# Performance work log

Hardware: AMD Instinct MI355X
Metric: run time of the kernel (lower is better)

## Reference

```python
import jax, jax.numpy as jnp
import numpy as np

N = 10000        # nodes
E = 160000       # edges (avg degree 16)
IN = 8 * 144     # 1152
OUT = 2 * 144    # 288 per ChebConv
KS = [4, 5, 6, 7]


def setup_inputs() -> dict:
    key = jax.random.key(0)
    ks = jax.random.split(key, 10)
    x = jax.random.normal(ks[0], (N, IN), dtype=jnp.float32)
    edge_index = jax.random.randint(ks[1], (2, E), 0, N, dtype=jnp.int32)
    d = {"x": x, "edge_index": edge_index}
    for i, (name, K) in enumerate(zip(["3", "5", "7", "9"], KS)):
        d["W" + name] = jax.random.normal(ks[2 + i], (K, IN, OUT), dtype=jnp.float32) * 0.02
        d["b" + name] = jnp.zeros((OUT,), dtype=jnp.float32)
    return d


def _cheb_basis(x, edge_index, K):
    """Chebyshev basis T_0..T_{K-1} of L_hat = -D^{-1/2} A D^{-1/2} (lambda_max=2,
    as in PyG ChebConv default; self-loop term 2/lambda_max - 1 = 0)."""
    row, col = edge_index[0], edge_index[1]  # source, target
    n = x.shape[0]
    w = jnp.ones(row.shape, x.dtype)
    deg = jax.ops.segment_sum(w, row, num_segments=n)
    dinv = jnp.where(deg > 0, jax.lax.rsqrt(jnp.maximum(deg, 1e-12)), 0.0)
    norm = -(dinv[row] * dinv[col])  # [E]

    def prop(h):  # out[i] = sum_{j->i} norm_e * h[j]
        return jax.ops.segment_sum(h[row] * norm[:, None], col, num_segments=n)

    Tx = [x, prop(x)]
    for _ in range(K - 2):
        Tx.append(2.0 * prop(Tx[-1]) - Tx[-2])
    return jnp.stack(Tx[:K], axis=0)  # [K, N, F]


def reference(x, edge_index, W3, b3, W5, b5, W7, b7, W9, b9):
    T = _cheb_basis(x, edge_index, max(KS))  # shared basis; identical math per conv
    outs = []
    for W, b in ((W3, b3), (W5, b5), (W7, b7), (W9, b9)):
        K = W.shape[0]
        outs.append(jnp.einsum('knf,kfo->no', T[:K], W) + b)
    return jnp.concatenate(outs, axis=1)  # [N, 4*OUT]
```

## Files before the change

### kernel.cpp

```cpp
#include <hip/hip_runtime.h>

#define NN 10000
#define NE 160000
#define FIN 1152
#define FOUT 288
#define FOUT_TOTAL 1152
#define NF (NN * FOUT)
#define WSL (FIN * FOUT)
#define NSLICE 22

typedef __attribute__((ext_vector_type(8))) short short8;
typedef __attribute__((ext_vector_type(8))) unsigned short ushort8v;
typedef __attribute__((ext_vector_type(4))) float floatx4;

__device__ __forceinline__ unsigned short f2bf(float f) {
  unsigned int u = __float_as_uint(f);
  u += 0x7FFF + ((u >> 16) & 1);
  return (unsigned short)(u >> 16);
}
__device__ __forceinline__ float bf2f(unsigned short u) {
  return __uint_as_float(((unsigned int)u) << 16);
}

__device__ __forceinline__ void async_copy16(void* lds, const void* gmem) {
  __builtin_amdgcn_global_load_lds(
      (const __attribute__((address_space(1))) unsigned int*)gmem,
      (__attribute__((address_space(3))) unsigned int*)lds, 16, 0, 0);
}


__global__ void deg_kernel(const int* __restrict__ ei, int* __restrict__ deg,
                           int* __restrict__ indeg) {
  int e = blockIdx.x * 256 + threadIdx.x;
  if (e < NE) {
    atomicAdd(&deg[ei[e]], 1);
    atomicAdd(&indeg[ei[NE + e]], 1);
  }
}

__global__ void dinv_kernel(const int* __restrict__ deg, float* __restrict__ dinv) {
  int i = blockIdx.x * 256 + threadIdx.x;
  if (i < NN) {
    int d = deg[i];
    dinv[i] = d > 0 ? rsqrtf((float)d) : 0.0f;
  }
}

__global__ void scan_kernel(const int* __restrict__ indeg, int* __restrict__ rowptr,
                            int* __restrict__ cursor) {
  __shared__ int s[256];
  __shared__ int carry_s;
  if (threadIdx.x == 0) carry_s = 0;
  __syncthreads();
  for (int base = 0; base < NN; base += 256) {
    int i = base + threadIdx.x;
    int v = (i < NN) ? indeg[i] : 0;
    s[threadIdx.x] = v;
    __syncthreads();
    for (int off = 1; off < 256; off <<= 1) {
      int t = (threadIdx.x >= off) ? s[threadIdx.x - off] : 0;
      __syncthreads();
      s[threadIdx.x] += t;
      __syncthreads();
    }
    int excl = s[threadIdx.x] - v + carry_s;
    if (i < NN) { rowptr[i] = excl; cursor[i] = excl; }
    __syncthreads();
    if (threadIdx.x == 0) carry_s += s[255];
    __syncthreads();
  }
  if (threadIdx.x == 0) rowptr[NN] = carry_s;
}

__global__ void scatter_kernel(const int* __restrict__ ei, const float* __restrict__ dinv,
                               int* __restrict__ cursor, int* __restrict__ srcarr,
                               float* __restrict__ wn) {
  int e = blockIdx.x * 256 + threadIdx.x;
  if (e < NE) {
    int r = ei[e], c = ei[NE + e];
    int pos = atomicAdd(&cursor[c], 1);
    srcarr[pos] = r;
    wn[pos] = -(dinv[r] * dinv[c]);
  }
}

__global__ void wtrans_kernel(const float* __restrict__ W0, const float* __restrict__ W1,
                              const float* __restrict__ W2, const float* __restrict__ W3,
                              unsigned short* __restrict__ Wt) {
  int i = blockIdx.x * 256 + threadIdx.x;
  if (i >= NSLICE * WSL) return;
  int s = i / WSL;
  int rem = i - s * WSL;
  int o = rem / FIN;
  int f = rem - o * FIN;
  int c, k;
  if (s < 4)       { c = 0; k = s; }
  else if (s < 9)  { c = 1; k = s - 4; }
  else if (s < 15) { c = 2; k = s - 9; }
  else             { c = 3; k = s - 15; }
  const float* W = (c == 0) ? W0 : (c == 1) ? W1 : (c == 2) ? W2 : W3;
  Wt[i] = f2bf(W[(size_t)k * WSL + (size_t)f * FOUT + o]);
}

__global__ void xcast_kernel(const float* __restrict__ x, unsigned short* __restrict__ xb) {
  int i = blockIdx.x * 256 + threadIdx.x;
  if (i < NN * FIN / 4) {
    float4 v = *(const float4*)(x + (size_t)i * 4);
    ushort4 r;
    r.x = f2bf(v.x); r.y = f2bf(v.y); r.z = f2bf(v.z); r.w = f2bf(v.w);
    *(ushort4*)(xb + (size_t)i * 4) = r;
  }
}

__global__ __launch_bounds__(256) void gemm_mfma_kernel(
    const unsigned short* __restrict__ Xb, const unsigned short* __restrict__ Wt,
    unsigned short* __restrict__ Yall) {
  const int bx = blockIdx.x;
  const int slice = bx / 3;
  const int n0 = (bx - slice * 3) * 96;
  const int m0 = blockIdx.y * 128;

  __shared__ unsigned short As[128][64];
  __shared__ unsigned short Bs[96][64];

  const int tid = threadIdx.x;
  const int lane = tid & 63;
  const int wave = tid >> 6;
  const int wx = wave & 1;
  const int wy = wave >> 1;
  const int lm = lane & 15;
  const int lkb = (lane >> 4) * 8;

  floatx4 acc[4][3];
#pragma unroll
  for (int i = 0; i < 4; i++)
#pragma unroll
    for (int j = 0; j < 3; j++) acc[i][j] = (floatx4){0.f, 0.f, 0.f, 0.f};

  const unsigned short* Wbase = Wt + (size_t)slice * WSL;

  for (int f0 = 0; f0 < FIN; f0 += 64) {
    __syncthreads();
#pragma unroll
    for (int i = 0; i < 4; i++) {
      int idx = i * 256 + tid;
      int row = idx >> 3;
      int cb = (idx & 7) * 16;
      int gr = m0 + row;
      gr = gr < NN ? gr : NN - 1;
      async_copy16((char*)&As[0][0] + idx * 16,
                   (const char*)Xb + ((size_t)gr * FIN + f0) * 2 + cb);
    }
#pragma unroll
    for (int i = 0; i < 3; i++) {
      int idx = i * 256 + tid;
      int row = idx >> 3;
      int cb = (idx & 7) * 16;
      async_copy16((char*)&Bs[0][0] + idx * 16,
                   (const char*)Wbase + ((size_t)(n0 + row) * FIN + f0) * 2 + cb);
    }
    __syncthreads();
#pragma unroll
    for (int s = 0; s < 2; s++) {
      short8 a[4], b[3];
#pragma unroll
      for (int i = 0; i < 4; i++)
        a[i] = *(const short8*)&As[wy * 64 + i * 16 + lm][s * 32 + lkb];
#pragma unroll
      for (int j = 0; j < 3; j++)
        b[j] = *(const short8*)&Bs[wx * 48 + j * 16 + lm][s * 32 + lkb];
#pragma unroll
      for (int i = 0; i < 4; i++)
#pragma unroll
        for (int j = 0; j < 3; j++)
          acc[i][j] = __builtin_amdgcn_mfma_f32_16x16x32_bf16(a[i], b[j], acc[i][j], 0, 0, 0);
    }
  }
  unsigned short* Yb = Yall + (size_t)slice * NF;
  const int cbase = n0 + wx * 48 + lm;
  const int rbase = (lane >> 4) * 4;
#pragma unroll
  for (int i = 0; i < 4; i++) {
#pragma unroll
    for (int r = 0; r < 4; r++) {
      int grow = m0 + wy * 64 + i * 16 + rbase + r;
      if (grow < NN) {
        unsigned short* op = Yb + (size_t)grow * FOUT + cbase;
#pragma unroll
        for (int j = 0; j < 3; j++) op[j * 16] = f2bf(acc[i][j][r]);
      }
    }
  }
}


struct StepArgs {
  const unsigned short* H[4];
  const unsigned short* Y[4];
  const unsigned short* P[4];
  unsigned short* D[4];
};

__global__ __launch_bounds__(576) void cl_step_kernel(
    StepArgs a, const int* __restrict__ rowptr, const int* __restrict__ srcarr,
    const float* __restrict__ wn) {
  const int slot = blockIdx.y;
  const unsigned short* __restrict__ H = a.H[slot];
  const int t = threadIdx.x;
  const int ln = t % 36;
  const int node = blockIdx.x * 16 + t / 36;
  if (node >= NN) return;
  const int off = ln * 8;
  const int rs = rowptr[node];
  const int re = rowptr[node + 1];
  float acc[8];
#pragma unroll
  for (int q = 0; q < 8; q++) acc[q] = 0.f;
  for (int p = rs; p < re; ++p) {
    int r = srcarr[p];
    float w = wn[p];
    ushort8v h = *(const ushort8v*)(H + (size_t)r * FOUT + off);
#pragma unroll
    for (int q = 0; q < 8; q++) acc[q] += w * bf2f(h[q]);
  }
  size_t o = (size_t)node * FOUT + off;
  ushort8v y = *(const ushort8v*)(a.Y[slot] + o);
  ushort8v d;
  if (a.P[slot]) {
    ushort8v pp = *(const ushort8v*)(a.P[slot] + o);
#pragma unroll
    for (int q = 0; q < 8; q++) d[q] = f2bf(bf2f(y[q]) + 2.f * acc[q] - bf2f(pp[q]));
  } else {
#pragma unroll
    for (int q = 0; q < 8; q++) d[q] = f2bf(bf2f(y[q]) + 2.f * acc[q]);
  }
  *(ushort8v*)(a.D[slot] + o) = d;
}

struct FinalArgs {
  const unsigned short* H[4];
  const unsigned short* Y[4];
  const unsigned short* P[4];
  const float* B[4];
  int conv[4];
};

__global__ __launch_bounds__(576) void cl_final_kernel(
    FinalArgs a, const int* __restrict__ rowptr, const int* __restrict__ srcarr,
    const float* __restrict__ wn, float* __restrict__ out) {
  const int slot = blockIdx.y;
  const unsigned short* __restrict__ H = a.H[slot];
  const int t = threadIdx.x;
  const int ln = t % 36;
  const int node = blockIdx.x * 16 + t / 36;
  if (node >= NN) return;
  const int off = ln * 8;
  const int rs = rowptr[node];
  const int re = rowptr[node + 1];
  float acc[8];
#pragma unroll
  for (int q = 0; q < 8; q++) acc[q] = 0.f;
  for (int p = rs; p < re; ++p) {
    int r = srcarr[p];
    float w = wn[p];
    ushort8v h = *(const ushort8v*)(H + (size_t)r * FOUT + off);
#pragma unroll
    for (int q = 0; q < 8; q++) acc[q] += w * bf2f(h[q]);
  }
  size_t o = (size_t)node * FOUT + off;
  ushort8v y = *(const ushort8v*)(a.Y[slot] + o);
  ushort8v pp = *(const ushort8v*)(a.P[slot] + o);
  const float* bias = a.B[slot] + off;
  float r8[8];
#pragma unroll
  for (int q = 0; q < 8; q++)
    r8[q] = bias[q] + bf2f(y[q]) + acc[q] - bf2f(pp[q]);
  float* op = out + (size_t)node * FOUT_TOTAL + a.conv[slot] * FOUT + off;
  *(float4*)(op + 0) = make_float4(r8[0], r8[1], r8[2], r8[3]);
  *(float4*)(op + 4) = make_float4(r8[4], r8[5], r8[6], r8[7]);
}


extern "C" void kernel_launch(void* const* d_in, const int* in_sizes, int n_in,
                              void* d_out, int out_size, void* d_ws, size_t ws_size,
                              hipStream_t stream) {
  const float* x = (const float*)d_in[0];
  const int* ei = (const int*)d_in[1];
  const float* W[4] = {(const float*)d_in[2], (const float*)d_in[4],
                       (const float*)d_in[6], (const float*)d_in[8]};
  const float* b[4] = {(const float*)d_in[3], (const float*)d_in[5],
                       (const float*)d_in[7], (const float*)d_in[9]};
  float* out = (float*)d_out;

  char* ws = (char*)d_ws;
  size_t off = 0;
  auto alloc = [&](size_t bytes) -> char* {
    char* p = ws + off;
    off += (bytes + 255) & ~(size_t)255;
    return p;
  };
  int* deg = (int*)alloc(NN * 4);
  int* indeg = (int*)alloc(NN * 4);
  int* rowptr = (int*)alloc((NN + 1) * 4);
  int* cursor = (int*)alloc(NN * 4);
  int* srcarr = (int*)alloc(NE * 4);
  float* wn = (float*)alloc(NE * 4);
  float* dinv = (float*)alloc(NN * 4);
  unsigned short* xb = (unsigned short*)alloc((size_t)NN * FIN * 2);
  unsigned short* Wt = (unsigned short*)alloc((size_t)NSLICE * WSL * 2);
  unsigned short* Yall = (unsigned short*)alloc((size_t)NSLICE * NF * 2);

  hipMemsetAsync(deg, 0, NN * 4, stream);
  hipMemsetAsync(indeg, 0, NN * 4, stream);

  deg_kernel<<<(NE + 255) / 256, 256, 0, stream>>>(ei, deg, indeg);
  dinv_kernel<<<(NN + 255) / 256, 256, 0, stream>>>(deg, dinv);
  scan_kernel<<<1, 256, 0, stream>>>(indeg, rowptr, cursor);
  scatter_kernel<<<(NE + 255) / 256, 256, 0, stream>>>(ei, dinv, cursor, srcarr, wn);
  wtrans_kernel<<<(NSLICE * WSL + 255) / 256, 256, 0, stream>>>(W[0], W[1], W[2], W[3], Wt);
  xcast_kernel<<<(NN * FIN / 4 + 255) / 256, 256, 0, stream>>>(x, xb);

  {
    dim3 grid(3 * NSLICE, (NN + 127) / 128);
    gemm_mfma_kernel<<<grid, 256, 0, stream>>>(xb, Wt, Yall);
  }

  const int nK[4] = {4, 5, 6, 7};
  const int st[4] = {0, 4, 9, 15};
  unsigned short* S[4];
  for (int c = 0; c < 4; c++) S[c] = xb + (size_t)c * NF;

  StepArgs sched[5];
  int nact[5] = {0, 0, 0, 0, 0};
  FinalArgs fa;

  for (int c = 3; c >= 0; c--) {
    int n = nK[c] - 1;
    int s0 = 6 - n;
    unsigned short* Yn = Yall + (size_t)(st[c] + n) * NF;
    unsigned short* A = S[c];
    for (int p = 1; p <= n; p++) {
      int s = s0 + p - 1;
      if (p < n) {
        unsigned short* H = (p & 1) ? Yn : A;
        unsigned short* D = (p & 1) ? A : Yn;
        int j = nact[s]++;
        sched[s].H[j] = H;
        sched[s].Y[j] = Yall + (size_t)(st[c] + n - p) * NF;
        sched[s].P[j] = (p == 1) ? nullptr : D;
        sched[s].D[j] = D;
      } else {
        int j = 3 - c;
        fa.H[j] = ((n - 1) & 1) ? A : Yn;
        fa.P[j] = ((n - 2) & 1) ? A : Yn;
        fa.Y[j] = Yall + (size_t)st[c] * NF;
        fa.B[j] = b[c];
        fa.conv[j] = c;
      }
    }
  }

  for (int s = 0; s < 5; s++) {
    cl_step_kernel<<<dim3(NN / 16, nact[s]), 576, 0, stream>>>(sched[s], rowptr, srcarr, wn);
  }
  cl_final_kernel<<<dim3(NN / 16, 4), 576, 0, stream>>>(fa, rowptr, srcarr, wn, out);
}
```

Baseline: 768.0 us.

## Swizzle GEMM LDS tiles and split propagation steps into 8 balanced column jobs

```diff
diff --git a/kernel.cpp b/kernel.cpp
--- a/kernel.cpp
+++ b/kernel.cpp
@@ -129,7 +129,7 @@
   const int wx = wave & 1;
   const int wy = wave >> 1;
   const int lm = lane & 15;
-  const int lkb = (lane >> 4) * 8;
+  const int hi = lane >> 4;
 
   floatx4 acc[4][3];
 #pragma unroll
@@ -145,30 +145,34 @@
     for (int i = 0; i < 4; i++) {
       int idx = i * 256 + tid;
       int row = idx >> 3;
-      int cb = (idx & 7) * 16;
+      int ck = idx & 7;
       int gr = m0 + row;
       gr = gr < NN ? gr : NN - 1;
       async_copy16((char*)&As[0][0] + idx * 16,
-                   (const char*)Xb + ((size_t)gr * FIN + f0) * 2 + cb);
+                   (const char*)Xb + ((size_t)gr * FIN + f0) * 2 + ((ck ^ (row & 7)) << 4));
     }
 #pragma unroll
     for (int i = 0; i < 3; i++) {
       int idx = i * 256 + tid;
       int row = idx >> 3;
-      int cb = (idx & 7) * 16;
+      int ck = idx & 7;
       async_copy16((char*)&Bs[0][0] + idx * 16,
-                   (const char*)Wbase + ((size_t)(n0 + row) * FIN + f0) * 2 + cb);
+                   (const char*)Wbase + ((size_t)(n0 + row) * FIN + f0) * 2 + ((ck ^ (row & 7)) << 4));
     }
     __syncthreads();
 #pragma unroll
     for (int s = 0; s < 2; s++) {
       short8 a[4], b[3];
 #pragma unroll
-      for (int i = 0; i < 4; i++)
-        a[i] = *(const short8*)&As[wy * 64 + i * 16 + lm][s * 32 + lkb];
-#pragma unroll
-      for (int j = 0; j < 3; j++)
-        b[j] = *(const short8*)&Bs[wx * 48 + j * 16 + lm][s * 32 + lkb];
+      for (int i = 0; i < 4; i++) {
+        int ar = wy * 64 + i * 16 + lm;
+        a[i] = *(const short8*)((const char*)&As[ar][0] + (((s * 4 + hi) ^ (ar & 7)) << 4));
+      }
+#pragma unroll
+      for (int j = 0; j < 3; j++) {
+        int br = wx * 48 + j * 16 + lm;
+        b[j] = *(const short8*)((const char*)&Bs[br][0] + (((s * 4 + hi) ^ (br & 7)) << 4));
+      }
 #pragma unroll
       for (int i = 0; i < 4; i++)
 #pragma unroll
@@ -194,25 +198,31 @@
 }
 
 
-struct StepArgs {
-  const unsigned short* H[4];
-  const unsigned short* Y[4];
-  const unsigned short* P[4];
-  unsigned short* D[4];
+struct Job {
+  const unsigned short* H;
+  const unsigned short* Y;
+  const unsigned short* P;
+  unsigned short* D;
+  int goff, gcnt;
 };
+struct JobArgs { Job j[8]; };
 
 __global__ __launch_bounds__(576) void cl_step_kernel(
-    StepArgs a, const int* __restrict__ rowptr, const int* __restrict__ srcarr,
+    JobArgs a, const int* __restrict__ rowptr, const int* __restrict__ srcarr,
     const float* __restrict__ wn) {
-  const int slot = blockIdx.y;
-  const unsigned short* __restrict__ H = a.H[slot];
+  const int job = blockIdx.x & 7;
+  const int nb = blockIdx.x >> 3;
+  const Job J = a.j[job];
+  const int g = J.gcnt;
+  const int npb = 576 / g;
   const int t = threadIdx.x;
-  const int ln = t % 36;
-  const int node = blockIdx.x * 16 + t / 36;
+  if (t >= npb * g) return;
+  const int node = nb * npb + t / g;
   if (node >= NN) return;
-  const int off = ln * 8;
+  const int off = (J.goff + t % g) * 8;
   const int rs = rowptr[node];
   const int re = rowptr[node + 1];
+  const unsigned short* __restrict__ H = J.H;
   float acc[8];
 #pragma unroll
   for (int q = 0; q < 8; q++) acc[q] = 0.f;
@@ -224,39 +234,44 @@
     for (int q = 0; q < 8; q++) acc[q] += w * bf2f(h[q]);
   }
   size_t o = (size_t)node * FOUT + off;
-  ushort8v y = *(const ushort8v*)(a.Y[slot] + o);
+  ushort8v y = *(const ushort8v*)(J.Y + o);
   ushort8v d;
-  if (a.P[slot]) {
-    ushort8v pp = *(const ushort8v*)(a.P[slot] + o);
+  if (J.P) {
+    ushort8v pp = *(const ushort8v*)(J.P + o);
 #pragma unroll
     for (int q = 0; q < 8; q++) d[q] = f2bf(bf2f(y[q]) + 2.f * acc[q] - bf2f(pp[q]));
   } else {
 #pragma unroll
     for (int q = 0; q < 8; q++) d[q] = f2bf(bf2f(y[q]) + 2.f * acc[q]);
   }
-  *(ushort8v*)(a.D[slot] + o) = d;
-}
-
-struct FinalArgs {
-  const unsigned short* H[4];
-  const unsigned short* Y[4];
-  const unsigned short* P[4];
-  const float* B[4];
-  int conv[4];
+  *(ushort8v*)(J.D + o) = d;
+}
+
+struct FJob {
+  const unsigned short* H;
+  const unsigned short* Y;
+  const unsigned short* P;
+  const float* B;
+  int conv, goff, gcnt;
 };
+struct FJobArgs { FJob j[8]; };
 
 __global__ __launch_bounds__(576) void cl_final_kernel(
-    FinalArgs a, const int* __restrict__ rowptr, const int* __restrict__ srcarr,
+    FJobArgs a, const int* __restrict__ rowptr, const int* __restrict__ srcarr,
     const float* __restrict__ wn, float* __restrict__ out) {
-  const int slot = blockIdx.y;
-  const unsigned short* __restrict__ H = a.H[slot];
+  const int job = blockIdx.x & 7;
+  const int nb = blockIdx.x >> 3;
+  const FJob J = a.j[job];
+  const int g = J.gcnt;
+  const int npb = 576 / g;
   const int t = threadIdx.x;
-  const int ln = t % 36;
-  const int node = blockIdx.x * 16 + t / 36;
+  if (t >= npb * g) return;
+  const int node = nb * npb + t / g;
   if (node >= NN) return;
-  const int off = ln * 8;
+  const int off = (J.goff + t % g) * 8;
   const int rs = rowptr[node];
   const int re = rowptr[node + 1];
+  const unsigned short* __restrict__ H = J.H;
   float acc[8];
 #pragma unroll
   for (int q = 0; q < 8; q++) acc[q] = 0.f;
@@ -268,14 +283,14 @@
     for (int q = 0; q < 8; q++) acc[q] += w * bf2f(h[q]);
   }
   size_t o = (size_t)node * FOUT + off;
-  ushort8v y = *(const ushort8v*)(a.Y[slot] + o);
-  ushort8v pp = *(const ushort8v*)(a.P[slot] + o);
-  const float* bias = a.B[slot] + off;
+  ushort8v y = *(const ushort8v*)(J.Y + o);
+  ushort8v pp = *(const ushort8v*)(J.P + o);
+  const float* bias = J.B + off;
   float r8[8];
 #pragma unroll
   for (int q = 0; q < 8; q++)
     r8[q] = bias[q] + bf2f(y[q]) + acc[q] - bf2f(pp[q]);
-  float* op = out + (size_t)node * FOUT_TOTAL + a.conv[slot] * FOUT + off;
+  float* op = out + (size_t)node * FOUT_TOTAL + J.conv * FOUT + off;
   *(float4*)(op + 0) = make_float4(r8[0], r8[1], r8[2], r8[3]);
   *(float4*)(op + 4) = make_float4(r8[4], r8[5], r8[6], r8[7]);
 }
@@ -330,9 +345,22 @@
   unsigned short* S[4];
   for (int c = 0; c < 4; c++) S[c] = xb + (size_t)c * NF;
 
-  StepArgs sched[5];
+  struct Slot {
+    const unsigned short* H;
+    const unsigned short* Y;
+    const unsigned short* P;
+    unsigned short* D;
+  };
+  Slot sched[5][4];
   int nact[5] = {0, 0, 0, 0, 0};
-  FinalArgs fa;
+  struct FSlot {
+    const unsigned short* H;
+    const unsigned short* Y;
+    const unsigned short* P;
+    const float* B;
+    int conv;
+  };
+  FSlot fs[4];
 
   for (int c = 3; c >= 0; c--) {
     int n = nK[c] - 1;
@@ -345,23 +373,60 @@
         unsigned short* H = (p & 1) ? Yn : A;
         unsigned short* D = (p & 1) ? A : Yn;
         int j = nact[s]++;
-        sched[s].H[j] = H;
-        sched[s].Y[j] = Yall + (size_t)(st[c] + n - p) * NF;
-        sched[s].P[j] = (p == 1) ? nullptr : D;
-        sched[s].D[j] = D;
+        sched[s][j].H = H;
+        sched[s][j].Y = Yall + (size_t)(st[c] + n - p) * NF;
+        sched[s][j].P = (p == 1) ? nullptr : D;
+        sched[s][j].D = D;
       } else {
         int j = 3 - c;
-        fa.H[j] = ((n - 1) & 1) ? A : Yn;
-        fa.P[j] = ((n - 2) & 1) ? A : Yn;
-        fa.Y[j] = Yall + (size_t)st[c] * NF;
-        fa.B[j] = b[c];
-        fa.conv[j] = c;
+        fs[j].H = ((n - 1) & 1) ? A : Yn;
+        fs[j].P = ((n - 2) & 1) ? A : Yn;
+        fs[j].Y = Yall + (size_t)st[c] * NF;
+        fs[j].B = b[c];
+        fs[j].conv = c;
       }
     }
   }
 
+  auto nb_for = [](int g) { int npb = 576 / g; return (NN + npb - 1) / npb; };
+
   for (int s = 0; s < 5; s++) {
-    cl_step_kernel<<<dim3(NN / 16, nact[s]), 576, 0, stream>>>(sched[s], rowptr, srcarr, wn);
-  }
-  cl_final_kernel<<<dim3(NN / 16, 4), 576, 0, stream>>>(fa, rowptr, srcarr, wn, out);
-}
+    int n = nact[s];
+    int slts[8], offs[8], cnts[8];
+    if (n == 1) {
+      const int cs[8] = {5, 5, 5, 5, 4, 4, 4, 4};
+      int o = 0;
+      for (int k = 0; k < 8; k++) { slts[k] = 0; offs[k] = o; cnts[k] = cs[k]; o += cs[k]; }
+    } else if (n == 2) {
+      for (int k = 0; k < 8; k++) { slts[k] = k >> 2; offs[k] = (k & 3) * 9; cnts[k] = 9; }
+    } else if (n == 3) {
+      int k = 0;
+      for (int sl = 0; sl < 2; sl++)
+        for (int i = 0; i < 3; i++) { slts[k] = sl; offs[k] = i * 12; cnts[k] = 12; k++; }
+      for (int i = 0; i < 2; i++) { slts[k] = 2; offs[k] = i * 18; cnts[k] = 18; k++; }
+    } else {
+      for (int k = 0; k < 8; k++) { slts[k] = k >> 1; offs[k] = (k & 1) * 18; cnts[k] = 18; }
+    }
+    JobArgs ja;
+    int maxNB = 0;
+    for (int k = 0; k < 8; k++) {
+      const Slot& sl = sched[s][slts[k]];
+      ja.j[k].H = sl.H; ja.j[k].Y = sl.Y; ja.j[k].P = sl.P; ja.j[k].D = sl.D;
+      ja.j[k].goff = offs[k]; ja.j[k].gcnt = cnts[k];
+      int nb = nb_for(cnts[k]);
+      if (nb > maxNB) maxNB = nb;
+    }
+    cl_step_kernel<<<8 * maxNB, 576, 0, stream>>>(ja, rowptr, srcarr, wn);
+  }
+
+  {
+    FJobArgs fja;
+    for (int k = 0; k < 8; k++) {
+      const FSlot& f = fs[k >> 1];
+      fja.j[k].H = f.H; fja.j[k].Y = f.Y; fja.j[k].P = f.P; fja.j[k].B = f.B;
+      fja.j[k].conv = f.conv;
+      fja.j[k].goff = (k & 1) * 18; fja.j[k].gcnt = 18;
+    }
+    cl_final_kernel<<<8 * nb_for(18), 576, 0, stream>>>(fja, rowptr, srcarr, wn, out);
+  }
+}
```

After: 766.4 us. Within noise of the previous version (-0.2%).

## Swizzle GEMM LDS layout and fuse per-conv Clenshaw steps into one gather pass

Applied to the files above, without the earlier changes.

```diff
diff --git a/kernel.cpp b/kernel.cpp
--- a/kernel.cpp
+++ b/kernel.cpp
@@ -129,7 +129,7 @@
   const int wx = wave & 1;
   const int wy = wave >> 1;
   const int lm = lane & 15;
-  const int lkb = (lane >> 4) * 8;
+  const int hi = lane >> 4;
 
   floatx4 acc[4][3];
 #pragma unroll
@@ -145,30 +145,34 @@
     for (int i = 0; i < 4; i++) {
       int idx = i * 256 + tid;
       int row = idx >> 3;
-      int cb = (idx & 7) * 16;
+      int ck = idx & 7;
       int gr = m0 + row;
       gr = gr < NN ? gr : NN - 1;
       async_copy16((char*)&As[0][0] + idx * 16,
-                   (const char*)Xb + ((size_t)gr * FIN + f0) * 2 + cb);
+                   (const char*)Xb + ((size_t)gr * FIN + f0) * 2 + ((ck ^ (row & 7)) << 4));
     }
 #pragma unroll
     for (int i = 0; i < 3; i++) {
       int idx = i * 256 + tid;
       int row = idx >> 3;
-      int cb = (idx & 7) * 16;
+      int ck = idx & 7;
       async_copy16((char*)&Bs[0][0] + idx * 16,
-                   (const char*)Wbase + ((size_t)(n0 + row) * FIN + f0) * 2 + cb);
+                   (const char*)Wbase + ((size_t)(n0 + row) * FIN + f0) * 2 + ((ck ^ (row & 7)) << 4));
     }
     __syncthreads();
 #pragma unroll
     for (int s = 0; s < 2; s++) {
       short8 a[4], b[3];
 #pragma unroll
-      for (int i = 0; i < 4; i++)
-        a[i] = *(const short8*)&As[wy * 64 + i * 16 + lm][s * 32 + lkb];
-#pragma unroll
-      for (int j = 0; j < 3; j++)
-        b[j] = *(const short8*)&Bs[wx * 48 + j * 16 + lm][s * 32 + lkb];
+      for (int i = 0; i < 4; i++) {
+        int ar = wy * 64 + i * 16 + lm;
+        a[i] = *(const short8*)((const char*)&As[ar][0] + (((s * 4 + hi) ^ (ar & 7)) << 4));
+      }
+#pragma unroll
+      for (int j = 0; j < 3; j++) {
+        int br = wx * 48 + j * 16 + lm;
+        b[j] = *(const short8*)((const char*)&Bs[br][0] + (((s * 4 + hi) ^ (br & 7)) << 4));
+      }
 #pragma unroll
       for (int i = 0; i < 4; i++)
 #pragma unroll
@@ -194,18 +198,17 @@
 }
 
 
-struct StepArgs {
+struct StepA {
   const unsigned short* H[4];
   const unsigned short* Y[4];
   const unsigned short* P[4];
   unsigned short* D[4];
 };
 
-__global__ __launch_bounds__(576) void cl_step_kernel(
-    StepArgs a, const int* __restrict__ rowptr, const int* __restrict__ srcarr,
+template <int NACT>
+__global__ __launch_bounds__(576) void cl_step_fused(
+    StepA a, const int* __restrict__ rowptr, const int* __restrict__ srcarr,
     const float* __restrict__ wn) {
-  const int slot = blockIdx.y;
-  const unsigned short* __restrict__ H = a.H[slot];
   const int t = threadIdx.x;
   const int ln = t % 36;
   const int node = blockIdx.x * 16 + t / 36;
@@ -213,31 +216,61 @@
   const int off = ln * 8;
   const int rs = rowptr[node];
   const int re = rowptr[node + 1];
-  float acc[8];
-#pragma unroll
-  for (int q = 0; q < 8; q++) acc[q] = 0.f;
-  for (int p = rs; p < re; ++p) {
+  float acc[NACT][8];
+#pragma unroll
+  for (int s = 0; s < NACT; s++)
+#pragma unroll
+    for (int q = 0; q < 8; q++) acc[s][q] = 0.f;
+
+  constexpr int U = (NACT <= 2) ? 4 : 2;
+  int p = rs;
+  for (; p + U <= re; p += U) {
+    int r[U];
+    float w[U];
+#pragma unroll
+    for (int u = 0; u < U; u++) { r[u] = srcarr[p + u]; w[u] = wn[p + u]; }
+    ushort8v h[U][NACT];
+#pragma unroll
+    for (int u = 0; u < U; u++)
+#pragma unroll
+      for (int s = 0; s < NACT; s++)
+        h[u][s] = *(const ushort8v*)(a.H[s] + (size_t)r[u] * FOUT + off);
+#pragma unroll
+    for (int u = 0; u < U; u++)
+#pragma unroll
+      for (int s = 0; s < NACT; s++)
+#pragma unroll
+        for (int q = 0; q < 8; q++) acc[s][q] += w[u] * bf2f(h[u][s][q]);
+  }
+  for (; p < re; ++p) {
     int r = srcarr[p];
     float w = wn[p];
-    ushort8v h = *(const ushort8v*)(H + (size_t)r * FOUT + off);
-#pragma unroll
-    for (int q = 0; q < 8; q++) acc[q] += w * bf2f(h[q]);
-  }
+#pragma unroll
+    for (int s = 0; s < NACT; s++) {
+      ushort8v hh = *(const ushort8v*)(a.H[s] + (size_t)r * FOUT + off);
+#pragma unroll
+      for (int q = 0; q < 8; q++) acc[s][q] += w * bf2f(hh[q]);
+    }
+  }
+
   size_t o = (size_t)node * FOUT + off;
-  ushort8v y = *(const ushort8v*)(a.Y[slot] + o);
-  ushort8v d;
-  if (a.P[slot]) {
-    ushort8v pp = *(const ushort8v*)(a.P[slot] + o);
-#pragma unroll
-    for (int q = 0; q < 8; q++) d[q] = f2bf(bf2f(y[q]) + 2.f * acc[q] - bf2f(pp[q]));
-  } else {
-#pragma unroll
-    for (int q = 0; q < 8; q++) d[q] = f2bf(bf2f(y[q]) + 2.f * acc[q]);
-  }
-  *(ushort8v*)(a.D[slot] + o) = d;
-}
-
-struct FinalArgs {
+#pragma unroll
+  for (int s = 0; s < NACT; s++) {
+    ushort8v y = *(const ushort8v*)(a.Y[s] + o);
+    ushort8v d;
+    if (a.P[s]) {
+      ushort8v pp = *(const ushort8v*)(a.P[s] + o);
+#pragma unroll
+      for (int q = 0; q < 8; q++) d[q] = f2bf(bf2f(y[q]) + 2.f * acc[s][q] - bf2f(pp[q]));
+    } else {
+#pragma unroll
+      for (int q = 0; q < 8; q++) d[q] = f2bf(bf2f(y[q]) + 2.f * acc[s][q]);
+    }
+    *(ushort8v*)(a.D[s] + o) = d;
+  }
+}
+
+struct FinalA {
   const unsigned short* H[4];
   const unsigned short* Y[4];
   const unsigned short* P[4];
@@ -245,11 +278,9 @@
   int conv[4];
 };
 
-__global__ __launch_bounds__(576) void cl_final_kernel(
-    FinalArgs a, const int* __restrict__ rowptr, const int* __restrict__ srcarr,
+__global__ __launch_bounds__(576) void cl_final_fused(
+    FinalA a, const int* __restrict__ rowptr, const int* __restrict__ srcarr,
     const float* __restrict__ wn, float* __restrict__ out) {
-  const int slot = blockIdx.y;
-  const unsigned short* __restrict__ H = a.H[slot];
   const int t = threadIdx.x;
   const int ln = t % 36;
   const int node = blockIdx.x * 16 + t / 36;
@@ -257,27 +288,57 @@
   const int off = ln * 8;
   const int rs = rowptr[node];
   const int re = rowptr[node + 1];
-  float acc[8];
-#pragma unroll
-  for (int q = 0; q < 8; q++) acc[q] = 0.f;
-  for (int p = rs; p < re; ++p) {
+  float acc[4][8];
+#pragma unroll
+  for (int s = 0; s < 4; s++)
+#pragma unroll
+    for (int q = 0; q < 8; q++) acc[s][q] = 0.f;
+
+  constexpr int U = 2;
+  int p = rs;
+  for (; p + U <= re; p += U) {
+    int r[U];
+    float w[U];
+#pragma unroll
+    for (int u = 0; u < U; u++) { r[u] = srcarr[p + u]; w[u] = wn[p + u]; }
+    ushort8v h[U][4];
+#pragma unroll
+    for (int u = 0; u < U; u++)
+#pragma unroll
+      for (int s = 0; s < 4; s++)
+        h[u][s] = *(const ushort8v*)(a.H[s] + (size_t)r[u] * FOUT + off);
+#pragma unroll
+    for (int u = 0; u < U; u++)
+#pragma unroll
+      for (int s = 0; s < 4; s++)
+#pragma unroll
+        for (int q = 0; q < 8; q++) acc[s][q] += w[u] * bf2f(h[u][s][q]);
+  }
+  for (; p < re; ++p) {
     int r = srcarr[p];
     float w = wn[p];
-    ushort8v h = *(const ushort8v*)(H + (size_t)r * FOUT + off);
-#pragma unroll
-    for (int q = 0; q < 8; q++) acc[q] += w * bf2f(h[q]);
-  }
+#pragma unroll
+    for (int s = 0; s < 4; s++) {
+      ushort8v hh = *(const ushort8v*)(a.H[s] + (size_t)r * FOUT + off);
+#pragma unroll
+      for (int q = 0; q < 8; q++) acc[s][q] += w * bf2f(hh[q]);
+    }
+  }
+
   size_t o = (size_t)node * FOUT + off;
-  ushort8v y = *(const ushort8v*)(a.Y[slot] + o);
-  ushort8v pp = *(const ushort8v*)(a.P[slot] + o);
-  const float* bias = a.B[slot] + off;
-  float r8[8];
-#pragma unroll
-  for (int q = 0; q < 8; q++)
-    r8[q] = bias[q] + bf2f(y[q]) + acc[q] - bf2f(pp[q]);
-  float* op = out + (size_t)node * FOUT_TOTAL + a.conv[slot] * FOUT + off;
-  *(float4*)(op + 0) = make_float4(r8[0], r8[1], r8[2], r8[3]);
-  *(float4*)(op + 4) = make_float4(r8[4], r8[5], r8[6], r8[7]);
+#pragma unroll
+  for (int s = 0; s < 4; s++) {
+    ushort8v y = *(const ushort8v*)(a.Y[s] + o);
+    ushort8v pp = *(const ushort8v*)(a.P[s] + o);
+    const float* bias = a.B[s] + off;
+    float r8[8];
+#pragma unroll
+    for (int q = 0; q < 8; q++)
+      r8[q] = bias[q] + bf2f(y[q]) + acc[s][q] - bf2f(pp[q]);
+    float* op = out + (size_t)node * FOUT_TOTAL + a.conv[s] * FOUT + off;
+    *(float4*)(op + 0) = make_float4(r8[0], r8[1], r8[2], r8[3]);
+    *(float4*)(op + 4) = make_float4(r8[4], r8[5], r8[6], r8[7]);
+  }
 }
 
 
@@ -330,9 +391,9 @@
   unsigned short* S[4];
   for (int c = 0; c < 4; c++) S[c] = xb + (size_t)c * NF;
 
-  StepArgs sched[5];
+  StepA sched[5];
   int nact[5] = {0, 0, 0, 0, 0};
-  FinalArgs fa;
+  FinalA fa;
 
   for (int c = 3; c >= 0; c--) {
     int n = nK[c] - 1;
@@ -360,8 +421,22 @@
     }
   }
 
+  for (int s = 0; s < 5; s++)
+    for (int j = nact[s]; j < 4; j++) {
+      sched[s].H[j] = sched[s].H[0];
+      sched[s].Y[j] = sched[s].Y[0];
+      sched[s].P[j] = sched[s].P[0];
+      sched[s].D[j] = sched[s].D[0];
+    }
+
+  const int grid_cl = NN / 16;
   for (int s = 0; s < 5; s++) {
-    cl_step_kernel<<<dim3(NN / 16, nact[s]), 576, 0, stream>>>(sched[s], rowptr, srcarr, wn);
-  }
-  cl_final_kernel<<<dim3(NN / 16, 4), 576, 0, stream>>>(fa, rowptr, srcarr, wn, out);
-}
+    switch (nact[s]) {
+      case 1: cl_step_fused<1><<<grid_cl, 576, 0, stream>>>(sched[s], rowptr, srcarr, wn); break;
+      case 2: cl_step_fused<2><<<grid_cl, 576, 0, stream>>>(sched[s], rowptr, srcarr, wn); break;
+      case 3: cl_step_fused<3><<<grid_cl, 576, 0, stream>>>(sched[s], rowptr, srcarr, wn); break;
+      default: cl_step_fused<4><<<grid_cl, 576, 0, stream>>>(sched[s], rowptr, srcarr, wn); break;
+    }
+  }
+  cl_final_fused<<<grid_cl, 576, 0, stream>>>(fa, rowptr, srcarr, wn, out);
+}
```

New measurement: 728.3 us. 5.2% less time.

## Stage feature-column slices of H in LDS for SpMM and swizzle GEMM LDS

Applied to the files above, without the earlier changes.

```diff
diff --git a/kernel.cpp b/kernel.cpp
--- a/kernel.cpp
+++ b/kernel.cpp
@@ -8,9 +8,10 @@
 #define NF (NN * FOUT)
 #define WSL (FIN * FOUT)
 #define NSLICE 22
+#define NGRAN 72
 
 typedef __attribute__((ext_vector_type(8))) short short8;
-typedef __attribute__((ext_vector_type(8))) unsigned short ushort8v;
+typedef __attribute__((ext_vector_type(4))) unsigned short ushort4v;
 typedef __attribute__((ext_vector_type(4))) float floatx4;
 
 __device__ __forceinline__ unsigned short f2bf(float f) {
@@ -129,7 +130,7 @@
   const int wx = wave & 1;
   const int wy = wave >> 1;
   const int lm = lane & 15;
-  const int lkb = (lane >> 4) * 8;
+  const int hi = lane >> 4;
 
   floatx4 acc[4][3];
 #pragma unroll
@@ -145,30 +146,34 @@
     for (int i = 0; i < 4; i++) {
       int idx = i * 256 + tid;
       int row = idx >> 3;
-      int cb = (idx & 7) * 16;
+      int ck = idx & 7;
       int gr = m0 + row;
       gr = gr < NN ? gr : NN - 1;
       async_copy16((char*)&As[0][0] + idx * 16,
-                   (const char*)Xb + ((size_t)gr * FIN + f0) * 2 + cb);
+                   (const char*)Xb + ((size_t)gr * FIN + f0) * 2 + ((ck ^ (row & 7)) << 4));
     }
 #pragma unroll
     for (int i = 0; i < 3; i++) {
       int idx = i * 256 + tid;
       int row = idx >> 3;
-      int cb = (idx & 7) * 16;
+      int ck = idx & 7;
       async_copy16((char*)&Bs[0][0] + idx * 16,
-                   (const char*)Wbase + ((size_t)(n0 + row) * FIN + f0) * 2 + cb);
+                   (const char*)Wbase + ((size_t)(n0 + row) * FIN + f0) * 2 + ((ck ^ (row & 7)) << 4));
     }
     __syncthreads();
 #pragma unroll
     for (int s = 0; s < 2; s++) {
       short8 a[4], b[3];
 #pragma unroll
-      for (int i = 0; i < 4; i++)
-        a[i] = *(const short8*)&As[wy * 64 + i * 16 + lm][s * 32 + lkb];
-#pragma unroll
-      for (int j = 0; j < 3; j++)
-        b[j] = *(const short8*)&Bs[wx * 48 + j * 16 + lm][s * 32 + lkb];
+      for (int i = 0; i < 4; i++) {
+        int ar = wy * 64 + i * 16 + lm;
+        a[i] = *(const short8*)((const char*)&As[ar][0] + (((s * 4 + hi) ^ (ar & 7)) << 4));
+      }
+#pragma unroll
+      for (int j = 0; j < 3; j++) {
+        int br = wx * 48 + j * 16 + lm;
+        b[j] = *(const short8*)((const char*)&Bs[br][0] + (((s * 4 + hi) ^ (br & 7)) << 4));
+      }
 #pragma unroll
       for (int i = 0; i < 4; i++)
 #pragma unroll
@@ -194,50 +199,72 @@
 }
 
 
-struct StepArgs {
+struct StepB {
   const unsigned short* H[4];
   const unsigned short* Y[4];
   const unsigned short* P[4];
   unsigned short* D[4];
 };
 
-__global__ __launch_bounds__(576) void cl_step_kernel(
-    StepArgs a, const int* __restrict__ rowptr, const int* __restrict__ srcarr,
+__global__ __launch_bounds__(576) void cl_step_lds(
+    StepB a, const int* __restrict__ rowptr, const int* __restrict__ srcarr,
     const float* __restrict__ wn) {
-  const int slot = blockIdx.y;
+  __shared__ unsigned short Hs[NN * 4];
+  const int slot = blockIdx.x / NGRAN;
+  const int g = blockIdx.x - slot * NGRAN;
+  const int off = g * 4;
   const unsigned short* __restrict__ H = a.H[slot];
   const int t = threadIdx.x;
-  const int ln = t % 36;
-  const int node = blockIdx.x * 16 + t / 36;
-  if (node >= NN) return;
-  const int off = ln * 8;
-  const int rs = rowptr[node];
-  const int re = rowptr[node + 1];
-  float acc[8];
-#pragma unroll
-  for (int q = 0; q < 8; q++) acc[q] = 0.f;
-  for (int p = rs; p < re; ++p) {
-    int r = srcarr[p];
-    float w = wn[p];
-    ushort8v h = *(const ushort8v*)(H + (size_t)r * FOUT + off);
-#pragma unroll
-    for (int q = 0; q < 8; q++) acc[q] += w * bf2f(h[q]);
-  }
-  size_t o = (size_t)node * FOUT + off;
-  ushort8v y = *(const ushort8v*)(a.Y[slot] + o);
-  ushort8v d;
-  if (a.P[slot]) {
-    ushort8v pp = *(const ushort8v*)(a.P[slot] + o);
-#pragma unroll
-    for (int q = 0; q < 8; q++) d[q] = f2bf(bf2f(y[q]) + 2.f * acc[q] - bf2f(pp[q]));
-  } else {
-#pragma unroll
-    for (int q = 0; q < 8; q++) d[q] = f2bf(bf2f(y[q]) + 2.f * acc[q]);
-  }
-  *(ushort8v*)(a.D[slot] + o) = d;
-}
-
-struct FinalArgs {
+
+  for (int i = t; i < NN; i += 576)
+    *(ushort4v*)&Hs[i * 4] = *(const ushort4v*)(H + (size_t)i * FOUT + off);
+  __syncthreads();
+
+  const unsigned short* __restrict__ Yp = a.Y[slot];
+  const unsigned short* __restrict__ Pp = a.P[slot];
+  unsigned short* __restrict__ Dp = a.D[slot];
+
+  for (int node = t; node < NN; node += 576) {
+    const int rs = rowptr[node];
+    const int re = rowptr[node + 1];
+    float acc[4] = {0.f, 0.f, 0.f, 0.f};
+    int p = rs;
+    for (; p + 4 <= re; p += 4) {
+      int r[4];
+      float w[4];
+#pragma unroll
+      for (int u = 0; u < 4; u++) { r[u] = srcarr[p + u]; w[u] = wn[p + u]; }
+      ushort4v h[4];
+#pragma unroll
+      for (int u = 0; u < 4; u++) h[u] = *(const ushort4v*)&Hs[r[u] * 4];
+#pragma unroll
+      for (int u = 0; u < 4; u++)
+#pragma unroll
+        for (int q = 0; q < 4; q++) acc[q] += w[u] * bf2f(h[u][q]);
+    }
+    for (; p < re; ++p) {
+      int r = srcarr[p];
+      float w = wn[p];
+      ushort4v h = *(const ushort4v*)&Hs[r * 4];
+#pragma unroll
+      for (int q = 0; q < 4; q++) acc[q] += w * bf2f(h[q]);
+    }
+    size_t o = (size_t)node * FOUT + off;
+    ushort4v y = *(const ushort4v*)(Yp + o);
+    ushort4v d;
+    if (Pp) {
+      ushort4v pp = *(const ushort4v*)(Pp + o);
+#pragma unroll
+      for (int q = 0; q < 4; q++) d[q] = f2bf(bf2f(y[q]) + 2.f * acc[q] - bf2f(pp[q]));
+    } else {
+#pragma unroll
+      for (int q = 0; q < 4; q++) d[q] = f2bf(bf2f(y[q]) + 2.f * acc[q]);
+    }
+    *(ushort4v*)(Dp + o) = d;
+  }
+}
+
+struct FinalB {
   const unsigned short* H[4];
   const unsigned short* Y[4];
   const unsigned short* P[4];
@@ -245,39 +272,60 @@
   int conv[4];
 };
 
-__global__ __launch_bounds__(576) void cl_final_kernel(
-    FinalArgs a, const int* __restrict__ rowptr, const int* __restrict__ srcarr,
+__global__ __launch_bounds__(576) void cl_final_lds(
+    FinalB a, const int* __restrict__ rowptr, const int* __restrict__ srcarr,
     const float* __restrict__ wn, float* __restrict__ out) {
-  const int slot = blockIdx.y;
+  __shared__ unsigned short Hs[NN * 4];
+  const int slot = blockIdx.x / NGRAN;
+  const int g = blockIdx.x - slot * NGRAN;
+  const int off = g * 4;
   const unsigned short* __restrict__ H = a.H[slot];
   const int t = threadIdx.x;
-  const int ln = t % 36;
-  const int node = blockIdx.x * 16 + t / 36;
-  if (node >= NN) return;
-  const int off = ln * 8;
-  const int rs = rowptr[node];
-  const int re = rowptr[node + 1];
-  float acc[8];
-#pragma unroll
-  for (int q = 0; q < 8; q++) acc[q] = 0.f;
-  for (int p = rs; p < re; ++p) {
-    int r = srcarr[p];
-    float w = wn[p];
-    ushort8v h = *(const ushort8v*)(H + (size_t)r * FOUT + off);
-#pragma unroll
-    for (int q = 0; q < 8; q++) acc[q] += w * bf2f(h[q]);
-  }
-  size_t o = (size_t)node * FOUT + off;
-  ushort8v y = *(const ushort8v*)(a.Y[slot] + o);
-  ushort8v pp = *(const ushort8v*)(a.P[slot] + o);
-  const float* bias = a.B[slot] + off;
-  float r8[8];
-#pragma unroll
-  for (int q = 0; q < 8; q++)
-    r8[q] = bias[q] + bf2f(y[q]) + acc[q] - bf2f(pp[q]);
-  float* op = out + (size_t)node * FOUT_TOTAL + a.conv[slot] * FOUT + off;
-  *(float4*)(op + 0) = make_float4(r8[0], r8[1], r8[2], r8[3]);
-  *(float4*)(op + 4) = make_float4(r8[4], r8[5], r8[6], r8[7]);
+
+  for (int i = t; i < NN; i += 576)
+    *(ushort4v*)&Hs[i * 4] = *(const ushort4v*)(H + (size_t)i * FOUT + off);
+  __syncthreads();
+
+  const unsigned short* __restrict__ Yp = a.Y[slot];
+  const unsigned short* __restrict__ Pp = a.P[slot];
+  const float* __restrict__ bias = a.B[slot] + off;
+  const int conv = a.conv[slot];
+
+  for (int node = t; node < NN; node += 576) {
+    const int rs = rowptr[node];
+    const int re = rowptr[node + 1];
+    float acc[4] = {0.f, 0.f, 0.f, 0.f};
+    int p = rs;
+    for (; p + 4 <= re; p += 4) {
+      int r[4];
+      float w[4];
+#pragma unroll
+      for (int u = 0; u < 4; u++) { r[u] = srcarr[p + u]; w[u] = wn[p + u]; }
+      ushort4v h[4];
+#pragma unroll
+      for (int u = 0; u < 4; u++) h[u] = *(const ushort4v*)&Hs[r[u] * 4];
+#pragma unroll
+      for (int u = 0; u < 4; u++)
+#pragma unroll
+        for (int q = 0; q < 4; q++) acc[q] += w[u] * bf2f(h[u][q]);
+    }
+    for (; p < re; ++p) {
+      int r = srcarr[p];
+      float w = wn[p];
+      ushort4v h = *(const ushort4v*)&Hs[r * 4];
+#pragma unroll
+      for (int q = 0; q < 4; q++) acc[q] += w * bf2f(h[q]);
+    }
+    size_t o = (size_t)node * FOUT + off;
+    ushort4v y = *(const ushort4v*)(Yp + o);
+    ushort4v pp = *(const ushort4v*)(Pp + o);
+    float r4[4];
+#pragma unroll
+    for (int q = 0; q < 4; q++)
+      r4[q] = bias[q] + bf2f(y[q]) + acc[q] - bf2f(pp[q]);
+    float* op = out + (size_t)node * FOUT_TOTAL + conv * FOUT + off;
+    *(float4*)op = make_float4(r4[0], r4[1], r4[2], r4[3]);
+  }
 }
 
 
@@ -330,9 +378,9 @@
   unsigned short* S[4];
   for (int c = 0; c < 4; c++) S[c] = xb + (size_t)c * NF;
 
-  StepArgs sched[5];
+  StepB sched[5];
   int nact[5] = {0, 0, 0, 0, 0};
-  FinalArgs fa;
+  FinalB fa;
 
   for (int c = 3; c >= 0; c--) {
     int n = nK[c] - 1;
@@ -360,8 +408,15 @@
     }
   }
 
-  for (int s = 0; s < 5; s++) {
-    cl_step_kernel<<<dim3(NN / 16, nact[s]), 576, 0, stream>>>(sched[s], rowptr, srcarr, wn);
-  }
-  cl_final_kernel<<<dim3(NN / 16, 4), 576, 0, stream>>>(fa, rowptr, srcarr, wn, out);
-}
+  for (int s = 0; s < 5; s++)
+    for (int j = nact[s]; j < 4; j++) {
+      sched[s].H[j] = sched[s].H[0];
+      sched[s].Y[j] = sched[s].Y[0];
+      sched[s].P[j] = sched[s].P[0];
+      sched[s].D[j] = sched[s].D[0];
+    }
+
+  for (int s = 0; s < 5; s++)
+    cl_step_lds<<<nact[s] * NGRAN, 576, 0, stream>>>(sched[s], rowptr, srcarr, wn);
+  cl_final_lds<<<4 * NGRAN, 576, 0, stream>>>(fa, rowptr, srcarr, wn, out);
+}
```

Measured after the change: 1.415 ms. +84.3%, slower.
